# Optimization experiments

Hardware: AMD Instinct MI355X
Metric: run time of the kernel (lower is better)

The kernel has to match this reference:

```python
import jax, jax.numpy as jnp
import numpy as np

ADDITIONAL_NOISE_STD = 0.1
RANDOM_MASK_FRACTION = 0.25
MASK_FILL_VALUE = 0.0


def setup_inputs() -> dict:
    key = jax.random.key(0)
    k1, k2, k3 = jax.random.split(key, 3)
    shape = (32, 1024, 2048)  # [batch, steps, obs_dim]
    data = jax.random.normal(k1, shape, dtype=jnp.float32)
    noise = jax.random.normal(k2, shape, dtype=jnp.float32)       # unit normal; scaled by std inside reference
    rand_vals = jax.random.uniform(k3, shape, dtype=jnp.float32)  # uniforms driving the topk mask
    return {"data": data, "noise": noise, "rand_vals": rand_vals}


def reference(data, noise, rand_vals):
    # apply_additional_noise: data + N(0, std)
    noisy = data + ADDITIONAL_NOISE_STD * noise

    # apply_random_mask along last dim:
    D = data.shape[-1]
    k = int(D * RANDOM_MASK_FRACTION)  # n_masked_per_step = 512
    _, idx = jax.lax.top_k(rand_vals, k)  # indices of k largest uniforms per row -> (B, S, k)

    # scatter True at topk indices (equivalent of torch scatter_ on a zero bool mask)
    B = data.shape[0] * data.shape[1]
    idx2 = idx.reshape(B, k)
    rows = jnp.arange(B)[:, None]
    mask = jnp.zeros((B, D), dtype=bool).at[rows, idx2].set(True).reshape(data.shape)

    masked = jnp.where(mask, jnp.asarray(MASK_FILL_VALUE, noisy.dtype), noisy)  # masked_fill
    mask_inverse = (~mask).astype(jnp.float32)  # logical_not(mask).float()
    return masked, mask_inverse
```

## Files before the change

kernel.cpp:

```cpp
#include <hip/hip_runtime.h>
#include <stdint.h>

#define D      2048
#define KSEL   512
#define CHUNKS 8

__device__ __forceinline__ int wave_sum_i(int v) {
    #pragma unroll
    for (int o = 32; o > 0; o >>= 1) v += __shfl_xor(v, o, 64);
    return v;
}
__device__ __forceinline__ unsigned wave_min_u(unsigned v) {
    #pragma unroll
    for (int o = 32; o > 0; o >>= 1) { unsigned t = __shfl_xor((int)v, o, 64); v = (t < v) ? t : v; }
    return v;
}
__device__ __forceinline__ unsigned wave_max_u(unsigned v) {
    #pragma unroll
    for (int o = 32; o > 0; o >>= 1) { unsigned t = __shfl_xor((int)v, o, 64); v = (t > v) ? t : v; }
    return v;
}

__device__ __forceinline__ int count_ge(const uint4* r, unsigned p) {
    int c = 0;
    #pragma unroll
    for (int i = 0; i < CHUNKS; ++i) {
        c += (r[i].x >= p) + (r[i].y >= p) + (r[i].z >= p) + (r[i].w >= p);
    }
    return wave_sum_i(c);
}
__device__ __forceinline__ int count_eq(const uint4* r, unsigned p) {
    int c = 0;
    #pragma unroll
    for (int i = 0; i < CHUNKS; ++i) {
        c += (r[i].x == p) + (r[i].y == p) + (r[i].z == p) + (r[i].w == p);
    }
    return wave_sum_i(c);
}
__device__ __forceinline__ unsigned min_ge(const uint4* r, unsigned lo) {
    unsigned m = 0xFFFFFFFFu;
    #pragma unroll
    for (int i = 0; i < CHUNKS; ++i) {
        unsigned a;
        a = r[i].x; if (a >= lo && a < m) m = a;
        a = r[i].y; if (a >= lo && a < m) m = a;
        a = r[i].z; if (a >= lo && a < m) m = a;
        a = r[i].w; if (a >= lo && a < m) m = a;
    }
    return wave_min_u(m);
}
__device__ __forceinline__ unsigned max_in(const uint4* r, unsigned lo, unsigned hi) {
    unsigned m = 0u;
    #pragma unroll
    for (int i = 0; i < CHUNKS; ++i) {
        unsigned a;
        a = r[i].x; if (a >= lo && a <= hi && a > m) m = a;
        a = r[i].y; if (a >= lo && a <= hi && a > m) m = a;
        a = r[i].z; if (a >= lo && a <= hi && a > m) m = a;
        a = r[i].w; if (a >= lo && a <= hi && a > m) m = a;
    }
    return wave_max_u(m);
}

__global__ __launch_bounds__(256)
void BaseObservationModel_42923903156755_kernel(
    const float* __restrict__ data, const float* __restrict__ noise,
    const float* __restrict__ rand_vals, float* __restrict__ out,
    long long n_elems)
{
    const int lane = threadIdx.x & 63;
    const long long rows = n_elems / D;
    const long long row  = (long long)blockIdx.x * 4 + (threadIdx.x >> 6);
    if (row >= rows) return;
    const long long base = row * D;

    const uint4*  rp = (const uint4*)(rand_vals + base);
    const float4* dp = (const float4*)(data + base);
    const float4* np = (const float4*)(noise + base);
    float4* op = (float4*)(out + base);
    float4* ip = (float4*)(out + n_elems + base);

    uint4  rb[CHUNKS];
    float4 dv[CHUNKS];
    float4 nv[CHUNKS];
    #pragma unroll
    for (int i = 0; i < CHUNKS; ++i) rb[i] = rp[i * 64 + lane];
    #pragma unroll
    for (int i = 0; i < CHUNKS; ++i) dv[i] = dp[i * 64 + lane];
    #pragma unroll
    for (int i = 0; i < CHUNKS; ++i) nv[i] = np[i * 64 + lane];

    unsigned lo = 0u, hi = 0x3F7FFFFFu;
    int cnt_lo = D, cnt_hi1 = 0;
    unsigned T; int need2; int cnteq;
    int it = 0;
    for (;;) {
        if (cnt_lo == KSEL) {
            T = min_ge(rb, lo);
            cnteq = count_eq(rb, T);
            need2 = cnteq;
            break;
        }
        if (cnt_hi1 == KSEL - 1) {
            T = max_in(rb, lo, hi);
            cnteq = count_eq(rb, T);
            need2 = 1;
            break;
        }
        if (lo == hi) {
            T = lo;
            cnteq = cnt_lo - cnt_hi1;
            need2 = KSEL - cnt_hi1;
            break;
        }
        unsigned mid;
        if (it & 1) {
            mid = lo + ((hi - lo + 1) >> 1);
        } else {
            float lof = __uint_as_float(lo);
            float hif = __uint_as_float(hi + 1);
            float frac = (float)(cnt_lo - KSEL) / (float)(cnt_lo - cnt_hi1);
            float mf = lof + frac * (hif - lof);
            mid = __float_as_uint(mf);
            if (mid < lo + 1) mid = lo + 1;
            if (mid > hi)     mid = hi;
        }
        int c = count_ge(rb, mid);
        if (c >= KSEL) { lo = mid; cnt_lo = c; }
        else           { hi = mid - 1; cnt_hi1 = c; }
        ++it;
    }

    const bool fast = (need2 == cnteq);
    int rank_base = 0;

    #pragma unroll
    for (int i = 0; i < CHUNKS; ++i) {
        const uint4 rv = rb[i];
        bool m0, m1, m2, m3;
        if (fast) {
            m0 = rv.x >= T; m1 = rv.y >= T; m2 = rv.z >= T; m3 = rv.w >= T;
        } else {
            const bool e0 = (rv.x == T), e1 = (rv.y == T), e2 = (rv.z == T), e3 = (rv.w == T);
            int myc = (int)e0 + (int)e1 + (int)e2 + (int)e3;
            int inc = myc;
            #pragma unroll
            for (int o = 1; o < 64; o <<= 1) {
                int t = __shfl_up(inc, o, 64);
                if (lane >= o) inc += t;
            }
            int r = rank_base + inc - myc;
            m0 = (rv.x > T) || (e0 && r < need2); r += (int)e0;
            m1 = (rv.y > T) || (e1 && r < need2); r += (int)e1;
            m2 = (rv.z > T) || (e2 && r < need2); r += (int)e2;
            m3 = (rv.w > T) || (e3 && r < need2); r += (int)e3;
            rank_base += __shfl(inc, 63, 64);
        }
        const float4 d = dv[i], n = nv[i];
        float4 o4, i4;
        o4.x = m0 ? 0.0f : fmaf(0.1f, n.x, d.x);
        o4.y = m1 ? 0.0f : fmaf(0.1f, n.y, d.y);
        o4.z = m2 ? 0.0f : fmaf(0.1f, n.z, d.z);
        o4.w = m3 ? 0.0f : fmaf(0.1f, n.w, d.w);
        i4.x = m0 ? 0.0f : 1.0f;
        i4.y = m1 ? 0.0f : 1.0f;
        i4.z = m2 ? 0.0f : 1.0f;
        i4.w = m3 ? 0.0f : 1.0f;
        op[i * 64 + lane] = o4;
        ip[i * 64 + lane] = i4;
    }
}

extern "C" void kernel_launch(void* const* d_in, const int* in_sizes, int n_in,
                              void* d_out, int out_size, void* d_ws, size_t ws_size,
                              hipStream_t stream) {
    const float* data      = (const float*)d_in[0];
    const float* noise     = (const float*)d_in[1];
    const float* rand_vals = (const float*)d_in[2];
    float* out = (float*)d_out;
    const long long n = (long long)in_sizes[0];
    const long long rows = n / D;
    const int blocks = (int)((rows + 3) / 4);
    BaseObservationModel_42923903156755_kernel<<<blocks, 256, 0, stream>>>(
        data, noise, rand_vals, out, n);
}
```

Measured before the change: 990.2 us.

## Stream data/noise with a two-chunk rolling prefetch and nontemporal loads/stores

Rather than holding all eight chunks of data and noise in registers, the kernel keeps only two chunks in flight and issues loads for chunk i+2 while writing chunk i. All global loads and stores now use nontemporal builtins, and launch bounds ask for 6 waves per SIMD to cut register pressure and raise occupancy. The aim is to lower VGPR use and overlap memory traffic with compute. The risk is that data/noise loads no longer overlap the top-k search phase, and nontemporal hints could change cache behaviour.

```diff
diff --git a/kernel.cpp b/kernel.cpp
--- a/kernel.cpp
+++ b/kernel.cpp
@@ -4,6 +4,9 @@
 #define D      2048
 #define KSEL   512
 #define CHUNKS 8
+
+typedef float    f4 __attribute__((ext_vector_type(4)));
+typedef unsigned u4 __attribute__((ext_vector_type(4)));
 
 __device__ __forceinline__ int wave_sum_i(int v) {
     #pragma unroll
@@ -21,48 +24,48 @@
     return v;
 }
 
-__device__ __forceinline__ int count_ge(const uint4* r, unsigned p) {
+__device__ __forceinline__ int count_ge(const u4* r, unsigned p) {
     int c = 0;
     #pragma unroll
     for (int i = 0; i < CHUNKS; ++i) {
-        c += (r[i].x >= p) + (r[i].y >= p) + (r[i].z >= p) + (r[i].w >= p);
+        c += (int)(r[i][0] >= p) + (int)(r[i][1] >= p) + (int)(r[i][2] >= p) + (int)(r[i][3] >= p);
     }
     return wave_sum_i(c);
 }
-__device__ __forceinline__ int count_eq(const uint4* r, unsigned p) {
+__device__ __forceinline__ int count_eq(const u4* r, unsigned p) {
     int c = 0;
     #pragma unroll
     for (int i = 0; i < CHUNKS; ++i) {
-        c += (r[i].x == p) + (r[i].y == p) + (r[i].z == p) + (r[i].w == p);
+        c += (int)(r[i][0] == p) + (int)(r[i][1] == p) + (int)(r[i][2] == p) + (int)(r[i][3] == p);
     }
     return wave_sum_i(c);
 }
-__device__ __forceinline__ unsigned min_ge(const uint4* r, unsigned lo) {
+__device__ __forceinline__ unsigned min_ge(const u4* r, unsigned lo) {
     unsigned m = 0xFFFFFFFFu;
     #pragma unroll
     for (int i = 0; i < CHUNKS; ++i) {
         unsigned a;
-        a = r[i].x; if (a >= lo && a < m) m = a;
-        a = r[i].y; if (a >= lo && a < m) m = a;
-        a = r[i].z; if (a >= lo && a < m) m = a;
-        a = r[i].w; if (a >= lo && a < m) m = a;
+        a = r[i][0]; if (a >= lo && a < m) m = a;
+        a = r[i][1]; if (a >= lo && a < m) m = a;
+        a = r[i][2]; if (a >= lo && a < m) m = a;
+        a = r[i][3]; if (a >= lo && a < m) m = a;
     }
     return wave_min_u(m);
 }
-__device__ __forceinline__ unsigned max_in(const uint4* r, unsigned lo, unsigned hi) {
+__device__ __forceinline__ unsigned max_in(const u4* r, unsigned lo, unsigned hi) {
     unsigned m = 0u;
     #pragma unroll
     for (int i = 0; i < CHUNKS; ++i) {
         unsigned a;
-        a = r[i].x; if (a >= lo && a <= hi && a > m) m = a;
-        a = r[i].y; if (a >= lo && a <= hi && a > m) m = a;
-        a = r[i].z; if (a >= lo && a <= hi && a > m) m = a;
-        a = r[i].w; if (a >= lo && a <= hi && a > m) m = a;
+        a = r[i][0]; if (a >= lo && a <= hi && a > m) m = a;
+        a = r[i][1]; if (a >= lo && a <= hi && a > m) m = a;
+        a = r[i][2]; if (a >= lo && a <= hi && a > m) m = a;
+        a = r[i][3]; if (a >= lo && a <= hi && a > m) m = a;
     }
     return wave_max_u(m);
 }
 
-__global__ __launch_bounds__(256)
+__global__ __launch_bounds__(256, 6)
 void BaseObservationModel_42923903156755_kernel(
     const float* __restrict__ data, const float* __restrict__ noise,
     const float* __restrict__ rand_vals, float* __restrict__ out,
@@ -74,21 +77,20 @@
     if (row >= rows) return;
     const long long base = row * D;
 
-    const uint4*  rp = (const uint4*)(rand_vals + base);
-    const float4* dp = (const float4*)(data + base);
-    const float4* np = (const float4*)(noise + base);
-    float4* op = (float4*)(out + base);
-    float4* ip = (float4*)(out + n_elems + base);
+    const u4* rp = (const u4*)(rand_vals + base);
+    const f4* dp = (const f4*)(data + base);
+    const f4* np = (const f4*)(noise + base);
+    f4* op = (f4*)(out + base);
+    f4* ip = (f4*)(out + n_elems + base);
 
-    uint4  rb[CHUNKS];
-    float4 dv[CHUNKS];
-    float4 nv[CHUNKS];
+    u4 rb[CHUNKS];
     #pragma unroll
-    for (int i = 0; i < CHUNKS; ++i) rb[i] = rp[i * 64 + lane];
-    #pragma unroll
-    for (int i = 0; i < CHUNKS; ++i) dv[i] = dp[i * 64 + lane];
-    #pragma unroll
-    for (int i = 0; i < CHUNKS; ++i) nv[i] = np[i * 64 + lane];
+    for (int i = 0; i < CHUNKS; ++i) rb[i] = __builtin_nontemporal_load(rp + i * 64 + lane);
+
+    f4 d0 = __builtin_nontemporal_load(dp + 0 * 64 + lane);
+    f4 n0 = __builtin_nontemporal_load(np + 0 * 64 + lane);
+    f4 d1 = __builtin_nontemporal_load(dp + 1 * 64 + lane);
+    f4 n1 = __builtin_nontemporal_load(np + 1 * 64 + lane);
 
     unsigned lo = 0u, hi = 0x3F7FFFFFu;
     int cnt_lo = D, cnt_hi1 = 0;
@@ -136,12 +138,18 @@
 
     #pragma unroll
     for (int i = 0; i < CHUNKS; ++i) {
-        const uint4 rv = rb[i];
+        f4 dn, nn;
+        if (i + 2 < CHUNKS) {
+            dn = __builtin_nontemporal_load(dp + (i + 2) * 64 + lane);
+            nn = __builtin_nontemporal_load(np + (i + 2) * 64 + lane);
+        }
+
+        const u4 rv = rb[i];
         bool m0, m1, m2, m3;
         if (fast) {
-            m0 = rv.x >= T; m1 = rv.y >= T; m2 = rv.z >= T; m3 = rv.w >= T;
+            m0 = rv[0] >= T; m1 = rv[1] >= T; m2 = rv[2] >= T; m3 = rv[3] >= T;
         } else {
-            const bool e0 = (rv.x == T), e1 = (rv.y == T), e2 = (rv.z == T), e3 = (rv.w == T);
+            const bool e0 = (rv[0] == T), e1 = (rv[1] == T), e2 = (rv[2] == T), e3 = (rv[3] == T);
             int myc = (int)e0 + (int)e1 + (int)e2 + (int)e3;
             int inc = myc;
             #pragma unroll
@@ -150,24 +158,28 @@
                 if (lane >= o) inc += t;
             }
             int r = rank_base + inc - myc;
-            m0 = (rv.x > T) || (e0 && r < need2); r += (int)e0;
-            m1 = (rv.y > T) || (e1 && r < need2); r += (int)e1;
-            m2 = (rv.z > T) || (e2 && r < need2); r += (int)e2;
-            m3 = (rv.w > T) || (e3 && r < need2); r += (int)e3;
+            m0 = (rv[0] > T) || (e0 && r < need2); r += (int)e0;
+            m1 = (rv[1] > T) || (e1 && r < need2); r += (int)e1;
+            m2 = (rv[2] > T) || (e2 && r < need2); r += (int)e2;
+            m3 = (rv[3] > T) || (e3 && r < need2); r += (int)e3;
             rank_base += __shfl(inc, 63, 64);
         }
-        const float4 d = dv[i], n = nv[i];
-        float4 o4, i4;
-        o4.x = m0 ? 0.0f : fmaf(0.1f, n.x, d.x);
-        o4.y = m1 ? 0.0f : fmaf(0.1f, n.y, d.y);
-        o4.z = m2 ? 0.0f : fmaf(0.1f, n.z, d.z);
-        o4.w = m3 ? 0.0f : fmaf(0.1f, n.w, d.w);
-        i4.x = m0 ? 0.0f : 1.0f;
-        i4.y = m1 ? 0.0f : 1.0f;
-        i4.z = m2 ? 0.0f : 1.0f;
-        i4.w = m3 ? 0.0f : 1.0f;
-        op[i * 64 + lane] = o4;
-        ip[i * 64 + lane] = i4;
+
+        const f4 d = d0, n = n0;
+        f4 o4, i4;
+        o4[0] = m0 ? 0.0f : fmaf(0.1f, n[0], d[0]);
+        o4[1] = m1 ? 0.0f : fmaf(0.1f, n[1], d[1]);
+        o4[2] = m2 ? 0.0f : fmaf(0.1f, n[2], d[2]);
+        o4[3] = m3 ? 0.0f : fmaf(0.1f, n[3], d[3]);
+        i4[0] = m0 ? 0.0f : 1.0f;
+        i4[1] = m1 ? 0.0f : 1.0f;
+        i4[2] = m2 ? 0.0f : 1.0f;
+        i4[3] = m3 ? 0.0f : 1.0f;
+        __builtin_nontemporal_store(o4, op + i * 64 + lane);
+        __builtin_nontemporal_store(i4, ip + i * 64 + lane);
+
+        d0 = d1; n0 = n1;
+        if (i + 2 < CHUNKS) { d1 = dn; n1 = nn; }
     }
 }
 
```

After: 968.9 us. -2.1%, faster.
